# Kernel optimization log

Hardware: AMD Instinct MI355X
Metric: run time of the kernel (lower is better)

The kernel has to match this reference:

```python
import jax, jax.numpy as jnp
import numpy as np

B, N, C_IN, C_MID, H, N_CLS = 128, 2048, 3, 64, 128, 40
EPS = 1e-5

def setup_inputs() -> dict:
    key = jax.random.key(0)
    ks = jax.random.split(key, 12)
    sc = lambda fan: 1.0 / np.sqrt(fan)
    return {
        "x": jax.random.normal(ks[0], (B, N, C_IN), jnp.float32),
        "conv_w": jax.random.normal(ks[1], (C_MID, C_IN), jnp.float32) * sc(C_IN),
        "conv_b": jnp.zeros((C_MID,), jnp.float32),
        "gamma": jnp.ones((C_MID,), jnp.float32),
        "beta": jnp.zeros((C_MID,), jnp.float32),
        "running_mean": jax.random.normal(ks[2], (C_MID,), jnp.float32) * 0.1,
        "running_var": jax.random.uniform(ks[3], (C_MID,), jnp.float32) + 0.5,
        "W_ih": jax.random.normal(ks[4], (4 * H, C_MID), jnp.float32) * sc(H),
        "W_hh": jax.random.normal(ks[5], (4 * H, H), jnp.float32) * sc(H),
        "b_ih": jax.random.normal(ks[6], (4 * H,), jnp.float32) * sc(H),
        "b_hh": jax.random.normal(ks[7], (4 * H,), jnp.float32) * sc(H),
        "W_out": jax.random.normal(ks[8], (N_CLS, H), jnp.float32) * sc(H),
        "b_out": jnp.zeros((N_CLS,), jnp.float32),
    }

def reference(x, conv_w, conv_b, gamma, beta, running_mean, running_var,
              W_ih, W_hh, b_ih, b_hh, W_out, b_out):
    # Conv1d(3,64,1) == per-point linear; BN (inference form) + ReLU.  [B,N,64]
    h = jnp.einsum('bnc,oc->bno', x, conv_w) + conv_b
    inv = gamma * jax.lax.rsqrt(running_var + EPS)
    h = jax.nn.relu((h - running_mean) * inv + beta)
    # Precompute input-side gate projections for all timesteps: [B,N,4H]
    xg = jnp.einsum('bnc,gc->bng', h, W_ih) + b_ih + b_hh
    Whh_T = W_hh.T  # [H,4H]

    def step(carry, xg_t):
        h_prev, c_prev = carry
        g = xg_t + h_prev @ Whh_T  # [B,4H]
        i, f, gg, o = jnp.split(g, 4, axis=-1)  # PyTorch gate order i,f,g,o
        i = jax.nn.sigmoid(i)
        f = jax.nn.sigmoid(f)
        gg = jnp.tanh(gg)
        o = jax.nn.sigmoid(o)
        c = f * c_prev + i * gg
        h_new = o * jnp.tanh(c)
        return (h_new, c), None

    init = (jnp.zeros((x.shape[0], W_hh.shape[1]), x.dtype),
            jnp.zeros((x.shape[0], W_hh.shape[1]), x.dtype))
    (h_last, _), _ = jax.lax.scan(step, init, jnp.swapaxes(xg, 0, 1))
    # Only the last timestep feeds the classifier head.
    return h_last @ W_out.T + b_out
```

## Files before the change

### kernel.cpp

```cpp
#include <hip/hip_runtime.h>
#include <math.h>

#define BB 128
#define NN 2048
#define CMID 64
#define HH 128
#define G4 512
#define NCLS 40
#define CH 64
#define NCH (NN / CH)
#define EPSV 1e-5f

__device__ __forceinline__ float fsigmoid(float x) {
    return 1.0f / (1.0f + __expf(-x));
}
__device__ __forceinline__ float ftanh2(float x) {
    return 2.0f / (1.0f + __expf(-2.0f * x)) - 1.0f;
}
__device__ __forceinline__ void fma4(float& a, const float4 w, const float4 v) {
    a = fmaf(w.x, v.x, a);
    a = fmaf(w.y, v.y, a);
    a = fmaf(w.z, v.z, a);
    a = fmaf(w.w, v.w, a);
}

__global__ __launch_bounds__(512, 1)
void lstm_seq_kernel(const float* __restrict__ x,
                     const float* __restrict__ conv_w, const float* __restrict__ conv_b,
                     const float* __restrict__ gamma,  const float* __restrict__ beta,
                     const float* __restrict__ rmean,  const float* __restrict__ rvar,
                     const float* __restrict__ W_ih,   const float* __restrict__ W_hh,
                     const float* __restrict__ b_ih,   const float* __restrict__ b_hh,
                     const float* __restrict__ W_out,  const float* __restrict__ b_out,
                     float* __restrict__ out)
{
    __shared__ float xg_s[CH][G4];
    __shared__ float hcT[CMID][CH];
    __shared__ float h_p[2][4][36];
    __shared__ float bias_s[G4];
    __shared__ float cf[4][CMID];

    const int t = threadIdx.x;
    const int b = blockIdx.x;
    const int j = t >> 2;
    const int s = t & 3;

    if (t < CMID) {
        float inv = gamma[t] * rsqrtf(rvar[t] + EPSV);
        cf[0][t] = conv_w[t * 3 + 0] * inv;
        cf[1][t] = conv_w[t * 3 + 1] * inv;
        cf[2][t] = conv_w[t * 3 + 2] * inv;
        cf[3][t] = (conv_b[t] - rmean[t]) * inv + beta[t];
    }
    bias_s[t] = b_ih[t] + b_hh[t];
    if (t < 2 * 4 * 36) ((float*)h_p)[t] = 0.0f;

    float4 whh[4][8];
    #pragma unroll
    for (int q = 0; q < 4; ++q) {
        const float* p = W_hh + (size_t)(q * HH + j) * HH + s * 32;
        #pragma unroll
        for (int i = 0; i < 8; ++i) whh[q][i] = *(const float4*)(p + 4 * i);
    }

    float c_reg = 0.0f;
    const float* xb = x + (size_t)b * NN * 3;

    for (int ch = 0; ch < NCH; ++ch) {
        const int base = ch * CH;
        __syncthreads();

        {
            const int n = t & 63;
            const int c0 = t >> 6;
            float x0 = xb[(base + n) * 3 + 0];
            float x1 = xb[(base + n) * 3 + 1];
            float x2 = xb[(base + n) * 3 + 2];
            #pragma unroll
            for (int i = 0; i < 8; ++i) {
                int c = i * 8 + c0;
                float hv = cf[3][c] + cf[0][c] * x0 + cf[1][c] * x1 + cf[2][c] * x2;
                hcT[c][n] = fmaxf(hv, 0.0f);
            }
        }
        __syncthreads();

        for (int pass = 0; pass < 2; ++pass) {
            const int r0 = (pass * 2 + 0) * HH + j;
            const int r1 = (pass * 2 + 1) * HH + j;
            float acc0[16], acc1[16];
            const float b0 = bias_s[r0], b1 = bias_s[r1];
            #pragma unroll
            for (int n = 0; n < 16; ++n) { acc0[n] = b0; acc1[n] = b1; }
            const float* w0p = W_ih + (size_t)r0 * CMID;
            const float* w1p = W_ih + (size_t)r1 * CMID;
            for (int k4 = 0; k4 < 16; ++k4) {
                float4 w0 = *(const float4*)(w0p + k4 * 4);
                float4 w1 = *(const float4*)(w1p + k4 * 4);
                const float* w0f = (const float*)&w0;
                const float* w1f = (const float*)&w1;
                #pragma unroll
                for (int kk = 0; kk < 4; ++kk) {
                    const int k = k4 * 4 + kk;
                    const float wa = w0f[kk];
                    const float wb = w1f[kk];
                    const float4* hc4 = (const float4*)&hcT[k][s * 16];
                    #pragma unroll
                    for (int i2 = 0; i2 < 4; ++i2) {
                        float4 hv = hc4[i2];
                        acc0[i2 * 4 + 0] = fmaf(wa, hv.x, acc0[i2 * 4 + 0]);
                        acc0[i2 * 4 + 1] = fmaf(wa, hv.y, acc0[i2 * 4 + 1]);
                        acc0[i2 * 4 + 2] = fmaf(wa, hv.z, acc0[i2 * 4 + 2]);
                        acc0[i2 * 4 + 3] = fmaf(wa, hv.w, acc0[i2 * 4 + 3]);
                        acc1[i2 * 4 + 0] = fmaf(wb, hv.x, acc1[i2 * 4 + 0]);
                        acc1[i2 * 4 + 1] = fmaf(wb, hv.y, acc1[i2 * 4 + 1]);
                        acc1[i2 * 4 + 2] = fmaf(wb, hv.z, acc1[i2 * 4 + 2]);
                        acc1[i2 * 4 + 3] = fmaf(wb, hv.w, acc1[i2 * 4 + 3]);
                    }
                }
            }
            #pragma unroll
            for (int n = 0; n < 16; ++n) {
                xg_s[s * 16 + n][r0] = acc0[n];
                xg_s[s * 16 + n][r1] = acc1[n];
            }
        }
        __syncthreads();

        for (int k = 0; k < CH; ++k) {
            const int p = (base + k) & 1;
            float a0, a1, a2, a3;
            if (s == 0) {
                a0 = xg_s[k][0 * HH + j];
                a1 = xg_s[k][1 * HH + j];
                a2 = xg_s[k][2 * HH + j];
                a3 = xg_s[k][3 * HH + j];
            } else {
                a0 = a1 = a2 = a3 = 0.0f;
            }
            const float4* hp = (const float4*)&h_p[p][s][0];
            #pragma unroll
            for (int i = 0; i < 8; ++i) {
                float4 hv = hp[i];
                fma4(a0, whh[0][i], hv);
                fma4(a1, whh[1][i], hv);
                fma4(a2, whh[2][i], hv);
                fma4(a3, whh[3][i], hv);
            }
            a0 += __shfl_xor(a0, 1); a0 += __shfl_xor(a0, 2);
            a1 += __shfl_xor(a1, 1); a1 += __shfl_xor(a1, 2);
            a2 += __shfl_xor(a2, 1); a2 += __shfl_xor(a2, 2);
            a3 += __shfl_xor(a3, 1); a3 += __shfl_xor(a3, 2);

            float gi = fsigmoid(a0);
            float gf = fsigmoid(a1);
            float gg = ftanh2(a2);
            float go = fsigmoid(a3);
            c_reg = gf * c_reg + gi * gg;
            float hv = go * ftanh2(c_reg);

            if (s == 0) h_p[p ^ 1][j >> 5][j & 31] = hv;
            __syncthreads();
        }
    }

    if (t < NCLS) {
        float acc = b_out[t];
        const float* wr = W_out + (size_t)t * HH;
        #pragma unroll
        for (int jj = 0; jj < HH; ++jj)
            acc = fmaf(wr[jj], h_p[0][jj >> 5][jj & 31], acc);
        out[(size_t)b * NCLS + t] = acc;
    }
}

extern "C" void kernel_launch(void* const* d_in, const int* in_sizes, int n_in,
                              void* d_out, int out_size, void* d_ws, size_t ws_size,
                              hipStream_t stream) {
    const float* x      = (const float*)d_in[0];
    const float* conv_w = (const float*)d_in[1];
    const float* conv_b = (const float*)d_in[2];
    const float* gamma  = (const float*)d_in[3];
    const float* beta   = (const float*)d_in[4];
    const float* rmean  = (const float*)d_in[5];
    const float* rvar   = (const float*)d_in[6];
    const float* W_ih   = (const float*)d_in[7];
    const float* W_hh   = (const float*)d_in[8];
    const float* b_ih   = (const float*)d_in[9];
    const float* b_hh   = (const float*)d_in[10];
    const float* W_out  = (const float*)d_in[11];
    const float* b_out  = (const float*)d_in[12];
    float* out = (float*)d_out;
    (void)d_ws; (void)ws_size; (void)in_sizes; (void)n_in; (void)out_size;

    lstm_seq_kernel<<<BB, 512, 0, stream>>>(x, conv_w, conv_b, gamma, beta,
                                            rmean, rvar, W_ih, W_hh, b_ih, b_hh,
                                            W_out, b_out, out);
}
```

Baseline: 2.137 ms.

## Keep half of W_hh in AGPRs and restructure input-gate projection per gate row

Loads the g and o gate rows of W_hh into accumulation registers (AGPRs) through inline asm. The i and f rows stay in regular VGPRs, with an explicit waves-per-EU attribute replacing launch_bounds. This relieves pressure on architectural VGPRs in the recurrent loop, so the compiler has room for the projection accumulators without spilling. The input projection now gives each thread one full gate row over a 32-step chunk (chunk size halved, with a padded hcT layout), and the xg term is added after the shuffle reduction rather than before. The cost is an AGPR read per weight element on every timestep, plus more chunk-boundary barriers.

```diff
diff --git a/kernel.cpp b/kernel.cpp
--- a/kernel.cpp
+++ b/kernel.cpp
@@ -7,9 +7,10 @@
 #define HH 128
 #define G4 512
 #define NCLS 40
-#define CH 64
+#define CH 32
 #define NCH (NN / CH)
 #define EPSV 1e-5f
+#define HPAD 36
 
 __device__ __forceinline__ float fsigmoid(float x) {
     return 1.0f / (1.0f + __expf(-x));
@@ -23,8 +24,17 @@
     a = fmaf(w.z, v.z, a);
     a = fmaf(w.w, v.w, a);
 }
-
-__global__ __launch_bounds__(512, 1)
+__device__ __forceinline__ void awrite(float& a, float v) {
+    asm volatile("v_accvgpr_write_b32 %0, %1" : "=a"(a) : "v"(v));
+}
+__device__ __forceinline__ float aread(const float& a) {
+    float v;
+    asm volatile("v_accvgpr_read_b32 %0, %1" : "=v"(v) : "a"(a));
+    return v;
+}
+
+__global__ __attribute__((amdgpu_flat_work_group_size(512, 512),
+                          amdgpu_waves_per_eu(2, 2)))
 void lstm_seq_kernel(const float* __restrict__ x,
                      const float* __restrict__ conv_w, const float* __restrict__ conv_b,
                      const float* __restrict__ gamma,  const float* __restrict__ beta,
@@ -34,11 +44,11 @@
                      const float* __restrict__ W_out,  const float* __restrict__ b_out,
                      float* __restrict__ out)
 {
-    __shared__ float xg_s[CH][G4];
-    __shared__ float hcT[CMID][CH];
-    __shared__ float h_p[2][4][36];
+    __shared__ float xg_s[CH][4][HH];
+    __shared__ float hcT[CMID][HPAD];
+    __shared__ float h_p[2][4][HPAD];
+    __shared__ float cf_s[4][CMID];
     __shared__ float bias_s[G4];
-    __shared__ float cf[4][CMID];
 
     const int t = threadIdx.x;
     const int b = blockIdx.x;
@@ -47,20 +57,29 @@
 
     if (t < CMID) {
         float inv = gamma[t] * rsqrtf(rvar[t] + EPSV);
-        cf[0][t] = conv_w[t * 3 + 0] * inv;
-        cf[1][t] = conv_w[t * 3 + 1] * inv;
-        cf[2][t] = conv_w[t * 3 + 2] * inv;
-        cf[3][t] = (conv_b[t] - rmean[t]) * inv + beta[t];
+        cf_s[0][t] = conv_w[t * 3 + 0] * inv;
+        cf_s[1][t] = conv_w[t * 3 + 1] * inv;
+        cf_s[2][t] = conv_w[t * 3 + 2] * inv;
+        cf_s[3][t] = (conv_b[t] - rmean[t]) * inv + beta[t];
     }
     bias_s[t] = b_ih[t] + b_hh[t];
-    if (t < 2 * 4 * 36) ((float*)h_p)[t] = 0.0f;
-
-    float4 whh[4][8];
+    if (t < 2 * 4 * HPAD) ((float*)h_p)[t] = 0.0f;
+
+    float4 whh_v[2][8];
     #pragma unroll
-    for (int q = 0; q < 4; ++q) {
-        const float* p = W_hh + (size_t)(q * HH + j) * HH + s * 32;
-        #pragma unroll
-        for (int i = 0; i < 8; ++i) whh[q][i] = *(const float4*)(p + 4 * i);
+    for (int i = 0; i < 8; ++i) {
+        whh_v[0][i] = *(const float4*)(W_hh + (size_t)(0 * HH + j) * HH + s * 32 + 4 * i);
+        whh_v[1][i] = *(const float4*)(W_hh + (size_t)(1 * HH + j) * HH + s * 32 + 4 * i);
+    }
+    float wa_g[32], wa_o[32];
+    #pragma unroll
+    for (int i = 0; i < 8; ++i) {
+        float4 wg = *(const float4*)(W_hh + (size_t)(2 * HH + j) * HH + s * 32 + 4 * i);
+        float4 wo = *(const float4*)(W_hh + (size_t)(3 * HH + j) * HH + s * 32 + 4 * i);
+        awrite(wa_g[4 * i + 0], wg.x); awrite(wa_g[4 * i + 1], wg.y);
+        awrite(wa_g[4 * i + 2], wg.z); awrite(wa_g[4 * i + 3], wg.w);
+        awrite(wa_o[4 * i + 0], wo.x); awrite(wa_o[4 * i + 1], wo.y);
+        awrite(wa_o[4 * i + 2], wo.z); awrite(wa_o[4 * i + 3], wo.w);
     }
 
     float c_reg = 0.0f;
@@ -71,86 +90,80 @@
         __syncthreads();
 
         {
-            const int n = t & 63;
-            const int c0 = t >> 6;
-            float x0 = xb[(base + n) * 3 + 0];
-            float x1 = xb[(base + n) * 3 + 1];
-            float x2 = xb[(base + n) * 3 + 2];
-            #pragma unroll
-            for (int i = 0; i < 8; ++i) {
-                int c = i * 8 + c0;
-                float hv = cf[3][c] + cf[0][c] * x0 + cf[1][c] * x1 + cf[2][c] * x2;
-                hcT[c][n] = fmaxf(hv, 0.0f);
+            const int c  = t & 63;
+            const int nb = t >> 6;
+            const float A0 = cf_s[0][c], A1 = cf_s[1][c];
+            const float A2 = cf_s[2][c], D0 = cf_s[3][c];
+            float4 hv;
+            #pragma unroll
+            for (int i = 0; i < 4; ++i) {
+                const int n = nb * 4 + i;
+                const float* xp = xb + (size_t)(base + n) * 3;
+                float r = D0 + A0 * xp[0] + A1 * xp[1] + A2 * xp[2];
+                ((float*)&hv)[i] = fmaxf(r, 0.0f);
             }
+            *(float4*)&hcT[c][nb * 4] = hv;
         }
         __syncthreads();
 
-        for (int pass = 0; pass < 2; ++pass) {
-            const int r0 = (pass * 2 + 0) * HH + j;
-            const int r1 = (pass * 2 + 1) * HH + j;
-            float acc0[16], acc1[16];
-            const float b0 = bias_s[r0], b1 = bias_s[r1];
-            #pragma unroll
-            for (int n = 0; n < 16; ++n) { acc0[n] = b0; acc1[n] = b1; }
-            const float* w0p = W_ih + (size_t)r0 * CMID;
-            const float* w1p = W_ih + (size_t)r1 * CMID;
+        {
+            const int q  = t >> 7;
+            const int jj = t & 127;
+            float acc[CH];
+            const float bv = bias_s[t];
+            #pragma unroll
+            for (int n = 0; n < CH; ++n) acc[n] = bv;
+            const float* wp = W_ih + (size_t)t * CMID;
             for (int k4 = 0; k4 < 16; ++k4) {
-                float4 w0 = *(const float4*)(w0p + k4 * 4);
-                float4 w1 = *(const float4*)(w1p + k4 * 4);
-                const float* w0f = (const float*)&w0;
-                const float* w1f = (const float*)&w1;
+                float4 w4 = *(const float4*)(wp + 4 * k4);
                 #pragma unroll
-                for (int kk = 0; kk < 4; ++kk) {
-                    const int k = k4 * 4 + kk;
-                    const float wa = w0f[kk];
-                    const float wb = w1f[kk];
-                    const float4* hc4 = (const float4*)&hcT[k][s * 16];
+                for (int e = 0; e < 4; ++e) {
+                    const int k = 4 * k4 + e;
+                    const float wv = ((const float*)&w4)[e];
+                    const float4* hr = (const float4*)&hcT[k][0];
                     #pragma unroll
-                    for (int i2 = 0; i2 < 4; ++i2) {
-                        float4 hv = hc4[i2];
-                        acc0[i2 * 4 + 0] = fmaf(wa, hv.x, acc0[i2 * 4 + 0]);
-                        acc0[i2 * 4 + 1] = fmaf(wa, hv.y, acc0[i2 * 4 + 1]);
-                        acc0[i2 * 4 + 2] = fmaf(wa, hv.z, acc0[i2 * 4 + 2]);
-                        acc0[i2 * 4 + 3] = fmaf(wa, hv.w, acc0[i2 * 4 + 3]);
-                        acc1[i2 * 4 + 0] = fmaf(wb, hv.x, acc1[i2 * 4 + 0]);
-                        acc1[i2 * 4 + 1] = fmaf(wb, hv.y, acc1[i2 * 4 + 1]);
-                        acc1[i2 * 4 + 2] = fmaf(wb, hv.z, acc1[i2 * 4 + 2]);
-                        acc1[i2 * 4 + 3] = fmaf(wb, hv.w, acc1[i2 * 4 + 3]);
+                    for (int n4 = 0; n4 < 8; ++n4) {
+                        float4 hv = hr[n4];
+                        acc[n4 * 4 + 0] = fmaf(wv, hv.x, acc[n4 * 4 + 0]);
+                        acc[n4 * 4 + 1] = fmaf(wv, hv.y, acc[n4 * 4 + 1]);
+                        acc[n4 * 4 + 2] = fmaf(wv, hv.z, acc[n4 * 4 + 2]);
+                        acc[n4 * 4 + 3] = fmaf(wv, hv.w, acc[n4 * 4 + 3]);
                     }
                 }
             }
             #pragma unroll
-            for (int n = 0; n < 16; ++n) {
-                xg_s[s * 16 + n][r0] = acc0[n];
-                xg_s[s * 16 + n][r1] = acc1[n];
-            }
+            for (int n = 0; n < CH; ++n) xg_s[n][q][jj] = acc[n];
         }
         __syncthreads();
 
         for (int k = 0; k < CH; ++k) {
-            const int p = (base + k) & 1;
-            float a0, a1, a2, a3;
-            if (s == 0) {
-                a0 = xg_s[k][0 * HH + j];
-                a1 = xg_s[k][1 * HH + j];
-                a2 = xg_s[k][2 * HH + j];
-                a3 = xg_s[k][3 * HH + j];
-            } else {
-                a0 = a1 = a2 = a3 = 0.0f;
-            }
+            const int p = k & 1;
+            float a0 = 0.f, a1 = 0.f, a2 = 0.f, a3 = 0.f;
             const float4* hp = (const float4*)&h_p[p][s][0];
             #pragma unroll
             for (int i = 0; i < 8; ++i) {
                 float4 hv = hp[i];
-                fma4(a0, whh[0][i], hv);
-                fma4(a1, whh[1][i], hv);
-                fma4(a2, whh[2][i], hv);
-                fma4(a3, whh[3][i], hv);
+                fma4(a0, whh_v[0][i], hv);
+                fma4(a1, whh_v[1][i], hv);
+                float t0, t1;
+                t0 = aread(wa_g[4 * i + 0]); t1 = aread(wa_o[4 * i + 0]);
+                a2 = fmaf(t0, hv.x, a2);     a3 = fmaf(t1, hv.x, a3);
+                t0 = aread(wa_g[4 * i + 1]); t1 = aread(wa_o[4 * i + 1]);
+                a2 = fmaf(t0, hv.y, a2);     a3 = fmaf(t1, hv.y, a3);
+                t0 = aread(wa_g[4 * i + 2]); t1 = aread(wa_o[4 * i + 2]);
+                a2 = fmaf(t0, hv.z, a2);     a3 = fmaf(t1, hv.z, a3);
+                t0 = aread(wa_g[4 * i + 3]); t1 = aread(wa_o[4 * i + 3]);
+                a2 = fmaf(t0, hv.w, a2);     a3 = fmaf(t1, hv.w, a3);
             }
             a0 += __shfl_xor(a0, 1); a0 += __shfl_xor(a0, 2);
             a1 += __shfl_xor(a1, 1); a1 += __shfl_xor(a1, 2);
             a2 += __shfl_xor(a2, 1); a2 += __shfl_xor(a2, 2);
             a3 += __shfl_xor(a3, 1); a3 += __shfl_xor(a3, 2);
+
+            a0 += xg_s[k][0][j];
+            a1 += xg_s[k][1][j];
+            a2 += xg_s[k][2][j];
+            a3 += xg_s[k][3][j];
 
             float gi = fsigmoid(a0);
             float gf = fsigmoid(a1);
```

Measured after the change: 3.002 ms. 40.5% more time.
